# Kernel optimization log

Hardware: AMD Instinct MI355X
Metric: run time of the kernel (lower is better)

The kernel has to match this reference:

```python
import jax, jax.numpy as jnp
import numpy as np

H = 32          # num attention heads
KVH = 8         # num key/value heads
D = 128         # head dim
THETA = 10000.0


def _rope_tables(kv_len):
    inv_freq = 1.0 / (THETA ** (jnp.arange(0, D, 2, dtype=jnp.float32) / D))  # [D/2]
    t = jnp.arange(kv_len, dtype=jnp.float32)
    freqs = jnp.outer(t, inv_freq)                  # [kv_len, D/2]
    emb = jnp.concatenate([freqs, freqs], axis=-1)  # [kv_len, D]
    return jnp.cos(emb), jnp.sin(emb)


def _rotate_half(x):
    x1, x2 = jnp.split(x, 2, axis=-1)
    return jnp.concatenate([-x2, x1], axis=-1)


def setup_inputs() -> dict:
    key = jax.random.key(0)
    ks = jax.random.split(key, 7)
    B, QL, KVL, HID = 4, 128, 4096, 4096
    hidden_states = jax.random.normal(ks[0], (B, QL, HID), jnp.float32)
    key_states = jax.random.normal(ks[1], (B, KVH, KVL, D), jnp.float32)
    value_states = jax.random.normal(ks[2], (B, KVH, KVL, D), jnp.float32)
    Wq = jax.random.normal(ks[3], (HID, H * D), jnp.float32) * (HID ** -0.5)
    Wo = jax.random.normal(ks[4], (H * D, HID), jnp.float32) * ((H * D) ** -0.5)
    position_ids = jnp.sort(jax.random.randint(ks[5], (B, KVL), 0, KVL), axis=-1).astype(jnp.int64)
    attention_mask = jax.random.randint(ks[6], (B, 1, QL, KVL), 0, 2) == 1
    return {"hidden_states": hidden_states, "key_states": key_states,
            "value_states": value_states, "Wq": Wq, "Wo": Wo,
            "position_ids": position_ids, "attention_mask": attention_mask}


def reference(hidden_states, key_states, value_states, Wq, Wo, position_ids, attention_mask):
    B, QL, HID = hidden_states.shape
    KVL = position_ids.shape[-1]

    # q projection -> [B, H, QL, D]
    q = (hidden_states @ Wq).reshape(B, QL, H, D).transpose(0, 2, 1, 3)

    # RoPE: apply rotation for the single max position per batch to all q positions
    cos, sin = _rope_tables(KVL)                               # [KVL, D]
    pos = jnp.take_along_axis(position_ids,
                              jnp.argmax(position_ids.astype(jnp.int32), axis=1)[:, None],
                              axis=1)                          # [B, 1]
    cos_b = cos[pos][:, None]                                  # [B, 1, 1, D]
    sin_b = sin[pos][:, None]
    q = q * cos_b + _rotate_half(q) * sin_b

    # GQA repeat kv heads -> [B, H, KVL, D]
    groups = H // KVH
    k = jnp.repeat(key_states, groups, axis=1)
    v = jnp.repeat(value_states, groups, axis=1)

    scores = jnp.einsum('bhqd,bhkd->bhqk', q, k) / jnp.sqrt(jnp.float32(D))
    scores = jnp.where(attention_mask, jnp.float32(-10000.0), scores)
    attn = jax.nn.softmax(scores.astype(jnp.float32), axis=-1).astype(q.dtype)

    out = jnp.einsum('bhqk,bhkd->bhqd', attn, v)               # [B, H, QL, D]
    out = out.transpose(0, 2, 1, 3).reshape(B, QL, H * D)
    return out @ Wo
```

## Files before the change

### kernel.cpp

```cpp
#include <hip/hip_runtime.h>
#include <math.h>

typedef __attribute__((ext_vector_type(8))) short bf16x8;
typedef __attribute__((ext_vector_type(4))) float f32x4;
typedef __attribute__((ext_vector_type(4))) short s16x4;
typedef __attribute__((ext_vector_type(4))) int i32x4;

__device__ inline unsigned short f2bf(float x){
  unsigned u = __builtin_bit_cast(unsigned, x);
  u = (u + 0x7FFFu + ((u >> 16) & 1u)) >> 16;
  return (unsigned short)u;
}
__device__ inline float bf2f(unsigned short v){
  return __builtin_bit_cast(float, (unsigned)v << 16);
}
__device__ inline unsigned pk2bf(float lo, float hi){
  return (unsigned)f2bf(lo) | ((unsigned)f2bf(hi) << 16);
}

__device__ inline void gl16(const void* g, void* l){
  __builtin_amdgcn_global_load_lds(
      (const __attribute__((address_space(1))) unsigned int*)g,
      (__attribute__((address_space(3))) unsigned int*)l, 16, 0, 0);
}

#define KVLEN 4096
#define QLEN  128
#define NH    32
#define NKVH  8
#define HD    128
#define HIDD  4096
#define NSPLIT 8
#define KVCHUNK (KVLEN / NSPLIT)

__global__ void prep_kernel(const int* __restrict__ pos32,
                            const unsigned int* __restrict__ mask32,
                            float* __restrict__ costab,
                            float* __restrict__ sintab,
                            int* __restrict__ flags){
  int tid = threadIdx.x;
  if (tid < 64){
    unsigned long long bal = __ballot((mask32[tid] & 0xFFFFFF00u) != 0);
    if (tid == 0) flags[0] = (bal != 0) ? 1 : 0;
  }
  int b = tid >> 6, j = tid & 63;
  bool pos64 = (pos32[2*4095 + 1] == 0);
  long long mpos;
  if (pos64) mpos = ((const long long*)pos32)[(size_t)b*KVLEN + KVLEN - 1];
  else       mpos = (long long)pos32[(size_t)b*KVLEN + KVLEN - 1];
  double inv = pow(10000.0, -((double)j) / 64.0);
  double ang = (double)mpos * inv;
  costab[b*64 + j] = (float)cos(ang);
  sintab[b*64 + j] = (float)sin(ang);
}

__global__ __launch_bounds__(256) void maskpack_kernel(const void* __restrict__ mask,
                                                       const int* __restrict__ flags,
                                                       unsigned long long* __restrict__ bits){
  int idx = blockIdx.x * 256 + threadIdx.x;
  bool m8 = (flags[0] != 0);
  bool v = m8 ? (((const unsigned char*)mask)[idx] != 0)
              : (((const int*)mask)[idx] != 0);
  unsigned long long bal = __ballot(v);
  if ((threadIdx.x & 63) == 0) bits[idx >> 6] = bal;
}

__global__ __launch_bounds__(256) void kvprep_kernel(const float* __restrict__ Kg,
                                                     const float* __restrict__ Vg,
                                                     const float* __restrict__ costab,
                                                     const float* __restrict__ sintab,
                                                     unsigned short* __restrict__ Kswz,
                                                     unsigned short* __restrict__ V2){
  __shared__ alignas(16) char tl[16384];
  int bid = blockIdx.x;
  int tid = threadIdx.x;
  int b = bid >> 9;
  const float* kin = Kg + (size_t)bid * 8192;
  const float* vin = Vg + (size_t)bid * 8192;
  unsigned short* kout = Kswz + (size_t)bid * 8192;
  unsigned short* vout = V2   + (size_t)bid * 8192;
#pragma unroll
  for (int i = 0; i < 4; ++i){
    int c = tid + 256*i;
    int r = c >> 4, d0 = (c & 15) * 8;
    int dp = d0 ^ 64;
    bool low = d0 < 64;
    f32x4 x0 = *(const f32x4*)(kin + r*128 + d0);
    f32x4 x1 = *(const f32x4*)(kin + r*128 + d0 + 4);
    f32x4 y0 = *(const f32x4*)(kin + r*128 + dp);
    f32x4 y1 = *(const f32x4*)(kin + r*128 + dp + 4);
    int j0 = d0 & 63;
    bf16x8 s;
#pragma unroll
    for (int t = 0; t < 4; ++t){
      float cc = costab[b*64 + j0 + t],     ss = sintab[b*64 + j0 + t];
      float c2 = costab[b*64 + j0 + 4 + t], s2 = sintab[b*64 + j0 + 4 + t];
      float v0 = low ? (x0[t]*cc + y0[t]*ss) : (x0[t]*cc - y0[t]*ss);
      float v1 = low ? (x1[t]*c2 + y1[t]*s2) : (x1[t]*c2 - y1[t]*s2);
      s[t] = (short)f2bf(v0);
      s[t+4] = (short)f2bf(v1);
    }
    unsigned o = ((unsigned)(r*256 + d0*2)) ^ (((unsigned)r & 7u) << 4);
    *(bf16x8*)(tl + o) = s;
  }
  __syncthreads();
#pragma unroll
  for (int i = 0; i < 4; ++i)
    *(bf16x8*)((char*)kout + tid*16 + i*4096) = *(const bf16x8*)(tl + tid*16 + i*4096);
#pragma unroll
  for (int i = 0; i < 4; ++i){
    int c = tid + 256*i;
    int l16 = c & 15, lk4 = (c >> 4) & 3, ks2 = (c >> 6) & 1, nf8 = c >> 7;
    int d = nf8*16 + l16;
    int kvb = ks2*32 + lk4*8;
    bf16x8 s;
#pragma unroll
    for (int e = 0; e < 8; ++e) s[e] = (short)f2bf(vin[(size_t)(kvb + e)*128 + d]);
    *(bf16x8*)(vout + (size_t)c*8) = s;
  }
}

__global__ __launch_bounds__(256) void wprep_kernel(const float* __restrict__ Wq,
                                                    const float* __restrict__ Wo,
                                                    const float* __restrict__ hidden,
                                                    unsigned short* __restrict__ WqImg,
                                                    unsigned short* __restrict__ WoImg,
                                                    unsigned short* __restrict__ A1img){
  __shared__ alignas(16) char tl[8192];
  int bid = blockIdx.x, tid = threadIdx.x;
  if (bid < 8192){
    const float* W = (bid < 4096) ? Wq : Wo;
    unsigned short* img = (bid < 4096) ? WqImg : WoImg;
    int t = bid & 4095;
    int bn = t >> 6, kt = t & 63;
    char* outB = (char*)img + (size_t)t * 8192;
#pragma unroll
    for (int i = 0; i < 2; ++i){
      int c = tid + 256*i;
      int n = c & 63, kc = c >> 6;
      const float* src = W + (size_t)(kt*64 + kc*8) * HIDD + bn*64 + n;
      bf16x8 s;
#pragma unroll
      for (int e = 0; e < 8; ++e) s[e] = (short)f2bf(src[(size_t)e * HIDD]);
      unsigned off = ((unsigned)(n*128 + kc*16)) ^ (((unsigned)n & 7u) << 4);
      *(bf16x8*)(tl + off) = s;
    }
    __syncthreads();
#pragma unroll
    for (int i = 0; i < 2; ++i)
      *(bf16x8*)(outB + tid*16 + i*4096) = *(const bf16x8*)(tl + tid*16 + i*4096);
  } else {
    int t = bid - 8192;
    int bm = t >> 6, kt = t & 63;
    char* outA = (char*)A1img + (size_t)t * 8192;
#pragma unroll
    for (int i = 0; i < 2; ++i){
      int c = tid + 256*i;
      int m = c >> 3, kc = c & 7;
      const float* src = hidden + (size_t)(bm*64 + m) * HIDD + kt*64 + kc*8;
      f32x4 x0 = *(const f32x4*)src;
      f32x4 x1 = *(const f32x4*)(src + 4);
      bf16x8 s;
#pragma unroll
      for (int e = 0; e < 4; ++e){ s[e] = (short)f2bf(x0[e]); s[e+4] = (short)f2bf(x1[e]); }
      unsigned off = ((unsigned)(m*128 + kc*16)) ^ (((unsigned)m & 7u) << 4);
      *(bf16x8*)(tl + off) = s;
    }
    __syncthreads();
#pragma unroll
    for (int i = 0; i < 2; ++i)
      *(bf16x8*)(outA + tid*16 + i*4096) = *(const bf16x8*)(tl + tid*16 + i*4096);
  }
}

template<int EPI>
__global__ __launch_bounds__(256, 2) void gemm_kernel(const unsigned short* __restrict__ Aimg,
                                                      const unsigned short* __restrict__ Bimg,
                                                      void* __restrict__ C_){
  __shared__ alignas(16) char smem[65536];
  int bid = blockIdx.x;
  int bn = (bid & 7) | ((bid >> 6) << 3);
  int bm = (bid >> 3) & 7;
  int tid = threadIdx.x, lane = tid & 63, w = tid >> 6;
  int wm = w >> 1, wn = w & 1;
  int l16 = lane & 15, lk4 = lane >> 4;
  const char* At = (const char*)Aimg + (size_t)(bm*64) * 8192;
  const char* Bt = (const char*)Bimg + (size_t)(bn*64) * 8192;
  f32x4 acc[2][2] = {};

#define GSTAGE(KT, BUF) do { \
    const char* ga_ = At + (size_t)(KT)*8192 + w*2048 + lane*16; \
    const char* gb_ = Bt + (size_t)(KT)*8192 + w*2048 + lane*16; \
    char* la_ = smem + (BUF)*16384 + w*2048; \
    char* lb_ = smem + (BUF)*16384 + 8192 + w*2048; \
    gl16(ga_, la_); gl16(ga_ + 1024, la_ + 1024); \
    gl16(gb_, lb_); gl16(gb_ + 1024, lb_ + 1024); \
  } while(0)

  GSTAGE(0, 0); GSTAGE(1, 1); GSTAGE(2, 2);

  for (int kt = 0; kt < 64; ++kt){
    if (kt < 62)      asm volatile("s_waitcnt vmcnt(8)" ::: "memory");
    else if (kt < 63) asm volatile("s_waitcnt vmcnt(4)" ::: "memory");
    else              asm volatile("s_waitcnt vmcnt(0)" ::: "memory");
    asm volatile("s_waitcnt lgkmcnt(0)" ::: "memory");
    __builtin_amdgcn_s_barrier();
    __builtin_amdgcn_sched_barrier(0);
    if (kt + 3 < 64) GSTAGE(kt + 3, (kt + 3) & 3);
    const char* Ab = smem + (kt & 3)*16384;
    const char* Bb = Ab + 8192;
    bf16x8 af[2][2], bfr[2][2];
#pragma unroll
    for (int i = 0; i < 2; ++i)
#pragma unroll
      for (int ks = 0; ks < 2; ++ks){
        unsigned m = (unsigned)(wm*32 + i*16 + l16);
        unsigned off = (m*128u + (unsigned)(ks*64 + lk4*16)) ^ ((m & 7u) << 4);
        af[i][ks] = *(const bf16x8*)(Ab + off);
      }
#pragma unroll
    for (int j = 0; j < 2; ++j)
#pragma unroll
      for (int ks = 0; ks < 2; ++ks){
        unsigned n = (unsigned)(wn*32 + j*16 + l16);
        unsigned off = (n*128u + (unsigned)(ks*64 + lk4*16)) ^ ((n & 7u) << 4);
        bfr[j][ks] = *(const bf16x8*)(Bb + off);
      }
#pragma unroll
    for (int i = 0; i < 2; ++i)
#pragma unroll
      for (int j = 0; j < 2; ++j)
#pragma unroll
        for (int ks = 0; ks < 2; ++ks)
          acc[i][j] = __builtin_amdgcn_mfma_f32_16x16x32_bf16(af[i][ks], bfr[j][ks], acc[i][j], 0, 0, 0);
  }
#undef GSTAGE

  if (EPI == 0){
    float* C = (float*)C_;
#pragma unroll
    for (int i = 0; i < 2; ++i)
#pragma unroll
      for (int j = 0; j < 2; ++j)
#pragma unroll
        for (int r = 0; r < 4; ++r){
          int row = bm*64 + wm*32 + i*16 + lk4*4 + r;
          int col = bn*64 + wn*32 + j*16 + l16;
          C[(size_t)row * HIDD + col] = acc[i][j][r];
        }
  } else {
    unsigned short* Q = (unsigned short*)C_;
    const float scale = 0.08838834764831845f * 1.4426950408889634f;
#pragma unroll
    for (int i = 0; i < 2; ++i)
#pragma unroll
      for (int j = 0; j < 2; ++j)
#pragma unroll
        for (int r = 0; r < 4; ++r){
          int row = bm*64 + wm*32 + i*16 + lk4*4 + r;
          int col = bn*64 + wn*32 + j*16 + l16;
          int b = row >> 7, ql = row & 127;
          int h = col >> 7, d = col & 127;
          Q[(((size_t)(b*NH + h)) * QLEN + ql) * HD + d] = f2bf(acc[i][j][r] * scale);
        }
  }
}

__global__ __launch_bounds__(256, 2) void attn_kernel(const unsigned short* __restrict__ Q,
                                                      const unsigned short* __restrict__ Kswz,
                                                      const unsigned short* __restrict__ V2,
                                                      const unsigned long long* __restrict__ bits,
                                                      unsigned short* __restrict__ Opart,
                                                      float* __restrict__ Mpart,
                                                      float* __restrict__ Lpart){
  __shared__ alignas(16) unsigned short Kbuf[2][8192];
  __shared__ alignas(16) unsigned short Vbuf[2][8192];
  int bid = blockIdx.x;
  int j = (bid >> 3) & 3;
  int g = (bid & 7) | ((bid >> 5) << 3);
  int s   = g & 7;
  int kvh = (g >> 3) & 7;
  int b   = g >> 6;
  int h   = kvh * 4 + j;

  int tid = threadIdx.x, lane = tid & 63, w = tid >> 6;
  int l16 = lane & 15, lk4 = lane >> 4;
  int lk4x4 = lk4 * 4;

  bf16x8 qf[2][4];
#pragma unroll
  for (int qg = 0; qg < 2; ++qg){
    const unsigned short* qp = Q + (((size_t)(b*NH + h) * QLEN) + w*32 + qg*16 + l16) * HD;
#pragma unroll
    for (int ks = 0; ks < 4; ++ks)
      qf[qg][ks] = *(const bf16x8*)(qp + ks*32 + lk4*8);
  }
  bf16x8 vone;
#pragma unroll
  for (int t = 0; t < 8; ++t) vone[t] = (short)0x3F80;

  f32x4 acc_o[2][8] = {};
  f32x4 acc_l[2] = {};
  float mrun[2] = {-1e30f, -1e30f};

  size_t kvhbase = (size_t)(b*NKVH + kvh) * (KVLEN/64);
  const unsigned short* Ktiles = Kswz + kvhbase * 8192;
  const unsigned short* Vtiles = V2   + kvhbase * 8192;
  size_t qrow0 = (size_t)(b*QLEN + w*32 + l16);

  const int t0 = s * (KVCHUNK/64), t1 = t0 + KVCHUNK/64;
  int srcb0 = (l16 + ((lk4 & 1) << 5)) << 2;
  int srcb1 = srcb0 + 64;

#define STAGE(T, BUF) do { \
    const char* gk_ = (const char*)(Ktiles + (size_t)(T)*8192) + w*4096 + lane*16; \
    const char* gv_ = (const char*)(Vtiles + (size_t)(T)*8192) + w*4096 + lane*16; \
    char* lk_ = (char*)(&Kbuf[BUF][0]) + w*4096; \
    char* lv_ = (char*)(&Vbuf[BUF][0]) + w*4096; \
    _Pragma("unroll") for (int i_ = 0; i_ < 4; ++i_) gl16(gk_ + i_*1024, lk_ + i_*1024); \
    _Pragma("unroll") for (int i_ = 0; i_ < 4; ++i_) gl16(gv_ + i_*1024, lv_ + i_*1024); \
  } while(0)

  STAGE(t0, 0);
  int cur = 0;
  for (int t = t0; t < t1; ++t){
    asm volatile("s_waitcnt vmcnt(0)" ::: "memory");
    asm volatile("s_waitcnt lgkmcnt(0)" ::: "memory");
    __builtin_amdgcn_s_barrier();
    __builtin_amdgcn_sched_barrier(0);
    if (t + 1 < t1) STAGE(t + 1, cur ^ 1);

    unsigned long long wrd[2];
    wrd[0] = bits[qrow0*64 + (size_t)t];
    wrd[1] = bits[(qrow0 + 16)*64 + (size_t)t];

    const char* Kc = (const char*)&Kbuf[cur][0];
    const char* Vc = (const char*)&Vbuf[cur][0];

    f32x4 sacc[2][4] = {};
#pragma unroll
    for (int nf = 0; nf < 4; ++nf){
      int krow = nf*16 + l16;
#pragma unroll
      for (int ks = 0; ks < 4; ++ks){
        unsigned byteoff = ((unsigned)krow*256u + (unsigned)(ks*32 + lk4*8)*2u) ^ (((unsigned)krow & 7u) << 4);
        bf16x8 kf = *(const bf16x8*)(Kc + byteoff);
        sacc[0][nf] = __builtin_amdgcn_mfma_f32_16x16x32_bf16(kf, qf[0][ks], sacc[0][nf], 0, 0, 0);
        sacc[1][nf] = __builtin_amdgcn_mfma_f32_16x16x32_bf16(kf, qf[1][ks], sacc[1][nf], 0, 0, 0);
      }
    }

    unsigned P32[2][8];
#pragma unroll
    for (int qg = 0; qg < 2; ++qg){
      float pp[4][4];
      float pm = -1e30f;
#pragma unroll
      for (int nf = 0; nf < 4; ++nf)
#pragma unroll
        for (int r = 0; r < 4; ++r){
          bool mk = (wrd[qg] >> (nf*16 + lk4x4 + r)) & 1ull;
          float sv = mk ? -20000.f : sacc[qg][nf][r];
          pp[nf][r] = sv;
          pm = fmaxf(pm, sv);
        }
      pm = fmaxf(pm, __shfl_xor(pm, 16, 64));
      pm = fmaxf(pm, __shfl_xor(pm, 32, 64));
      if (__any(pm > mrun[qg])){
        float mnew = fmaxf(mrun[qg], pm);
        float corr = exp2f(mrun[qg] - mnew);
        mrun[qg] = mnew;
#pragma unroll
        for (int nf8 = 0; nf8 < 8; ++nf8)
#pragma unroll
          for (int r = 0; r < 4; ++r) acc_o[qg][nf8][r] *= corr;
#pragma unroll
        for (int r = 0; r < 4; ++r) acc_l[qg][r] *= corr;
      }
#pragma unroll
      for (int nf = 0; nf < 4; ++nf){
        float e0 = exp2f(pp[nf][0] - mrun[qg]);
        float e1 = exp2f(pp[nf][1] - mrun[qg]);
        float e2 = exp2f(pp[nf][2] - mrun[qg]);
        float e3 = exp2f(pp[nf][3] - mrun[qg]);
        P32[qg][nf*2]     = pk2bf(e0, e1);
        P32[qg][nf*2 + 1] = pk2bf(e2, e3);
      }
    }

    bf16x8 pf[2][2];
    bool hi = lk4 >= 2;
#pragma unroll
    for (int qg = 0; qg < 2; ++qg)
#pragma unroll
      for (int ks2 = 0; ks2 < 2; ++ks2){
        int a0 = __builtin_amdgcn_ds_bpermute(srcb0, (int)P32[qg][ks2*4 + 0]);
        int b0 = __builtin_amdgcn_ds_bpermute(srcb0, (int)P32[qg][ks2*4 + 2]);
        int a1 = __builtin_amdgcn_ds_bpermute(srcb0, (int)P32[qg][ks2*4 + 1]);
        int b1 = __builtin_amdgcn_ds_bpermute(srcb0, (int)P32[qg][ks2*4 + 3]);
        int a2 = __builtin_amdgcn_ds_bpermute(srcb1, (int)P32[qg][ks2*4 + 0]);
        int b2 = __builtin_amdgcn_ds_bpermute(srcb1, (int)P32[qg][ks2*4 + 2]);
        int a3 = __builtin_amdgcn_ds_bpermute(srcb1, (int)P32[qg][ks2*4 + 1]);
        int b3 = __builtin_amdgcn_ds_bpermute(srcb1, (int)P32[qg][ks2*4 + 3]);
        i32x4 wv = { hi ? b0 : a0, hi ? b1 : a1, hi ? b2 : a2, hi ? b3 : a3 };
        pf[qg][ks2] = __builtin_bit_cast(bf16x8, wv);
      }

#pragma unroll
    for (int nf8 = 0; nf8 < 8; ++nf8)
#pragma unroll
      for (int ks2 = 0; ks2 < 2; ++ks2){
        unsigned byteoff = (unsigned)(nf8*2 + ks2)*1024u + (unsigned)lane*16u;
        bf16x8 vf = *(const bf16x8*)(Vc + byteoff);
        acc_o[0][nf8] = __builtin_amdgcn_mfma_f32_16x16x32_bf16(vf, pf[0][ks2], acc_o[0][nf8], 0, 0, 0);
        acc_o[1][nf8] = __builtin_amdgcn_mfma_f32_16x16x32_bf16(vf, pf[1][ks2], acc_o[1][nf8], 0, 0, 0);
      }
#pragma unroll
    for (int qg = 0; qg < 2; ++qg)
#pragma unroll
      for (int ks2 = 0; ks2 < 2; ++ks2)
        acc_l[qg] = __builtin_amdgcn_mfma_f32_16x16x32_bf16(vone, pf[qg][ks2], acc_l[qg], 0, 0, 0);

    cur ^= 1;
  }
#undef STAGE

  size_t rowbase = ((size_t)(s*4 + b) * NH + h) * QLEN + w*32 + l16;
#pragma unroll
  for (int qg = 0; qg < 2; ++qg){
    size_t row = rowbase + qg*16;
#pragma unroll
    for (int nf8 = 0; nf8 < 8; ++nf8){
      s16x4 o;
#pragma unroll
      for (int r = 0; r < 4; ++r) o[r] = (short)f2bf(acc_o[qg][nf8][r]);
      *(s16x4*)&Opart[row * HD + nf8*16 + lk4x4] = o;
    }
    if (lk4 == 0){
      Mpart[row] = mrun[qg];
      Lpart[row] = acc_l[qg][0];
    }
  }
}

__global__ __launch_bounds__(256) void combine_kernel(const unsigned short* __restrict__ Opart,
                                                      const float* __restrict__ Mpart,
                                                      const float* __restrict__ Lpart,
                                                      unsigned short* __restrict__ A2img){
  int idx = blockIdx.x * 256 + threadIdx.x;
  int d4 = idx & 31;
  int row = idx >> 5;
  const int RS = 4 * NH * QLEN;
  float m[NSPLIT];
  float M = -1e30f;
#pragma unroll
  for (int s = 0; s < NSPLIT; ++s){
    m[s] = Mpart[(size_t)s*RS + row];
    M = fmaxf(M, m[s]);
  }
  float L = 0.f;
  f32x4 num = {};
#pragma unroll
  for (int s = 0; s < NSPLIT; ++s){
    float wsc = exp2f(m[s] - M);
    L += wsc * Lpart[(size_t)s*RS + row];
    s16x4 o = *(const s16x4*)&Opart[((size_t)s*RS + row) * HD + d4*4];
#pragma unroll
    for (int t = 0; t < 4; ++t) num[t] += wsc * bf2f((unsigned short)o[t]);
  }
  int ql = row & 127, h = (row >> 7) & 31, b = row >> 12;
  int bm = b*2 + (ql >> 6), mm = ql & 63;
  int kt = h*2 + (d4 >> 4), kl = (d4*4) & 63;
  s16x4 res;
#pragma unroll
  for (int t = 0; t < 4; ++t) res[t] = (short)f2bf(num[t] / L);
  char* tile = (char*)A2img + (size_t)(bm*64 + kt) * 8192;
  unsigned off = ((unsigned)(mm*128 + kl*2)) ^ (((unsigned)mm & 7u) << 4);
  *(s16x4*)(tile + off) = res;
}

extern "C" void kernel_launch(void* const* d_in, const int* in_sizes, int n_in,
                              void* d_out, int out_size, void* d_ws, size_t ws_size,
                              hipStream_t stream){
  (void)in_sizes; (void)n_in; (void)out_size; (void)ws_size;
  const float* hidden = (const float*)d_in[0];
  const float* kst    = (const float*)d_in[1];
  const float* vst    = (const float*)d_in[2];
  const float* wq     = (const float*)d_in[3];
  const float* wo     = (const float*)d_in[4];
  const void*  pos    = d_in[5];
  const void*  mask   = d_in[6];
  float* out = (float*)d_out;

  char* ws = (char*)d_ws;
  unsigned short* Kswz  = (unsigned short*)ws;
  unsigned short* V2    = (unsigned short*)(ws + (32u << 20));
  unsigned short* WoImg = (unsigned short*)(ws + (64u << 20));
  unsigned short* WqImg = (unsigned short*)(ws + (96u << 20));
  unsigned short* Opart = (unsigned short*)(ws + (96u << 20));
  unsigned short* A1img = (unsigned short*)(ws + (128u << 20));
  unsigned short* qbf   = (unsigned short*)(ws + (132u << 20));
  unsigned short* A2img = (unsigned short*)(ws + (136u << 20));
  float* Mpart = (float*)(ws + (140u << 20));
  float* Lpart = (float*)(ws + (140u << 20) + (512u << 10));
  unsigned long long* bits = (unsigned long long*)(ws + (141u << 20));
  float* costab = (float*)(ws + (141u << 20) + (256u << 10));
  float* sintab = costab + 256;
  int*   flags  = (int*)(sintab + 256);

  prep_kernel<<<1, 256, 0, stream>>>((const int*)pos, (const unsigned int*)mask,
                                     costab, sintab, flags);
  maskpack_kernel<<<8192, 256, 0, stream>>>(mask, flags, bits);
  kvprep_kernel<<<2048, 256, 0, stream>>>(kst, vst, costab, sintab, Kswz, V2);
  wprep_kernel<<<8704, 256, 0, stream>>>(wq, wo, hidden, WqImg, WoImg, A1img);
  gemm_kernel<1><<<512, 256, 0, stream>>>(A1img, WqImg, qbf);
  attn_kernel<<<1024, 256, 0, stream>>>(qbf, Kswz, V2, bits, Opart, Mpart, Lpart);
  combine_kernel<<<2048, 256, 0, stream>>>(Opart, Mpart, Lpart, A2img);
  gemm_kernel<0><<<512, 256, 0, stream>>>(A2img, WoImg, out);
}
```

Before: 230.6 us.

## Fuse prep kernels into one launch, deepen GEMM k-step, halve attention splits

Merges the four preprocessing kernels (rope table, mask packing, K/V conversion, weight/hidden conversion) into a single launch, computing RoPE sin/cos inline per element instead of from a precomputed table. This removes several launch gaps and serial dependencies. The GEMM now double-buffers 128-wide k-tiles instead of triple/quad-buffering 64-wide ones, which halves the number of barriers but makes the prefetch shallower. The attention KV split count drops from 8 to 4, so fewer blocks and less partial-result traffic go into combine, at the cost of lower parallelism.

```diff
diff --git a/kernel.cpp b/kernel.cpp
--- a/kernel.cpp
+++ b/kernel.cpp
@@ -30,146 +30,128 @@
 #define NKVH  8
 #define HD    128
 #define HIDD  4096
-#define NSPLIT 8
+#define NSPLIT 4
 #define KVCHUNK (KVLEN / NSPLIT)
 
-__global__ void prep_kernel(const int* __restrict__ pos32,
-                            const unsigned int* __restrict__ mask32,
-                            float* __restrict__ costab,
-                            float* __restrict__ sintab,
-                            int* __restrict__ flags){
-  int tid = threadIdx.x;
-  if (tid < 64){
-    unsigned long long bal = __ballot((mask32[tid] & 0xFFFFFF00u) != 0);
-    if (tid == 0) flags[0] = (bal != 0) ? 1 : 0;
-  }
-  int b = tid >> 6, j = tid & 63;
-  bool pos64 = (pos32[2*4095 + 1] == 0);
-  long long mpos;
-  if (pos64) mpos = ((const long long*)pos32)[(size_t)b*KVLEN + KVLEN - 1];
-  else       mpos = (long long)pos32[(size_t)b*KVLEN + KVLEN - 1];
-  double inv = pow(10000.0, -((double)j) / 64.0);
-  double ang = (double)mpos * inv;
-  costab[b*64 + j] = (float)cos(ang);
-  sintab[b*64 + j] = (float)sin(ang);
-}
-
-__global__ __launch_bounds__(256) void maskpack_kernel(const void* __restrict__ mask,
-                                                       const int* __restrict__ flags,
-                                                       unsigned long long* __restrict__ bits){
-  int idx = blockIdx.x * 256 + threadIdx.x;
-  bool m8 = (flags[0] != 0);
-  bool v = m8 ? (((const unsigned char*)mask)[idx] != 0)
-              : (((const int*)mask)[idx] != 0);
-  unsigned long long bal = __ballot(v);
-  if ((threadIdx.x & 63) == 0) bits[idx >> 6] = bal;
-}
-
-__global__ __launch_bounds__(256) void kvprep_kernel(const float* __restrict__ Kg,
-                                                     const float* __restrict__ Vg,
-                                                     const float* __restrict__ costab,
-                                                     const float* __restrict__ sintab,
-                                                     unsigned short* __restrict__ Kswz,
-                                                     unsigned short* __restrict__ V2){
+__global__ __launch_bounds__(256) void prepall_kernel(
+    const float* __restrict__ Kg, const float* __restrict__ Vg,
+    const float* __restrict__ Wq, const float* __restrict__ Wo,
+    const float* __restrict__ hidden, const void* __restrict__ mask,
+    const int* __restrict__ pos32,
+    unsigned short* __restrict__ Kswz, unsigned short* __restrict__ V2,
+    unsigned short* __restrict__ WqImg, unsigned short* __restrict__ WoImg,
+    unsigned short* __restrict__ A1img,
+    unsigned long long* __restrict__ bits){
   __shared__ alignas(16) char tl[16384];
-  int bid = blockIdx.x;
-  int tid = threadIdx.x;
-  int b = bid >> 9;
-  const float* kin = Kg + (size_t)bid * 8192;
-  const float* vin = Vg + (size_t)bid * 8192;
-  unsigned short* kout = Kswz + (size_t)bid * 8192;
-  unsigned short* vout = V2   + (size_t)bid * 8192;
-#pragma unroll
-  for (int i = 0; i < 4; ++i){
-    int c = tid + 256*i;
-    int r = c >> 4, d0 = (c & 15) * 8;
-    int dp = d0 ^ 64;
-    bool low = d0 < 64;
-    f32x4 x0 = *(const f32x4*)(kin + r*128 + d0);
-    f32x4 x1 = *(const f32x4*)(kin + r*128 + d0 + 4);
-    f32x4 y0 = *(const f32x4*)(kin + r*128 + dp);
-    f32x4 y1 = *(const f32x4*)(kin + r*128 + dp + 4);
-    int j0 = d0 & 63;
-    bf16x8 s;
-#pragma unroll
-    for (int t = 0; t < 4; ++t){
-      float cc = costab[b*64 + j0 + t],     ss = sintab[b*64 + j0 + t];
-      float c2 = costab[b*64 + j0 + 4 + t], s2 = sintab[b*64 + j0 + 4 + t];
-      float v0 = low ? (x0[t]*cc + y0[t]*ss) : (x0[t]*cc - y0[t]*ss);
-      float v1 = low ? (x1[t]*c2 + y1[t]*s2) : (x1[t]*c2 - y1[t]*s2);
-      s[t] = (short)f2bf(v0);
-      s[t+4] = (short)f2bf(v1);
-    }
-    unsigned o = ((unsigned)(r*256 + d0*2)) ^ (((unsigned)r & 7u) << 4);
-    *(bf16x8*)(tl + o) = s;
-  }
-  __syncthreads();
-#pragma unroll
-  for (int i = 0; i < 4; ++i)
-    *(bf16x8*)((char*)kout + tid*16 + i*4096) = *(const bf16x8*)(tl + tid*16 + i*4096);
-#pragma unroll
-  for (int i = 0; i < 4; ++i){
-    int c = tid + 256*i;
-    int l16 = c & 15, lk4 = (c >> 4) & 3, ks2 = (c >> 6) & 1, nf8 = c >> 7;
-    int d = nf8*16 + l16;
-    int kvb = ks2*32 + lk4*8;
-    bf16x8 s;
-#pragma unroll
-    for (int e = 0; e < 8; ++e) s[e] = (short)f2bf(vin[(size_t)(kvb + e)*128 + d]);
-    *(bf16x8*)(vout + (size_t)c*8) = s;
-  }
-}
-
-__global__ __launch_bounds__(256) void wprep_kernel(const float* __restrict__ Wq,
-                                                    const float* __restrict__ Wo,
-                                                    const float* __restrict__ hidden,
-                                                    unsigned short* __restrict__ WqImg,
-                                                    unsigned short* __restrict__ WoImg,
-                                                    unsigned short* __restrict__ A1img){
-  __shared__ alignas(16) char tl[8192];
   int bid = blockIdx.x, tid = threadIdx.x;
+
   if (bid < 8192){
-    const float* W = (bid < 4096) ? Wq : Wo;
-    unsigned short* img = (bid < 4096) ? WqImg : WoImg;
-    int t = bid & 4095;
-    int bn = t >> 6, kt = t & 63;
-    char* outB = (char*)img + (size_t)t * 8192;
-#pragma unroll
-    for (int i = 0; i < 2; ++i){
+    const unsigned int* m32 = (const unsigned int*)mask;
+    unsigned long long det = __ballot((m32[tid & 63] & 0xFFFFFF00u) != 0);
+    bool m8 = (det != 0);
+    int idx = bid * 256 + tid;
+    bool v = m8 ? (((const unsigned char*)mask)[idx] != 0)
+                : (((const int*)mask)[idx] != 0);
+    unsigned long long bal = __ballot(v);
+    if ((tid & 63) == 0) bits[idx >> 6] = bal;
+
+  } else if (bid < 10240){
+    int t = bid - 8192;
+    int b = t >> 9;
+    const float* kin = Kg + (size_t)t * 8192;
+    const float* vin = Vg + (size_t)t * 8192;
+    unsigned short* kout = Kswz + (size_t)t * 8192;
+    unsigned short* vout = V2   + (size_t)t * 8192;
+    bool pos64 = (pos32[2*4095 + 1] == 0);
+    float mpos;
+    if (pos64) mpos = (float)((const long long*)pos32)[(size_t)b*KVLEN + KVLEN - 1];
+    else       mpos = (float)pos32[(size_t)b*KVLEN + KVLEN - 1];
+    const float KC = -0.2076205059298351f;
+#pragma unroll
+    for (int i = 0; i < 4; ++i){
       int c = tid + 256*i;
-      int n = c & 63, kc = c >> 6;
-      const float* src = W + (size_t)(kt*64 + kc*8) * HIDD + bn*64 + n;
+      int r = c >> 4, d0 = (c & 15) * 8;
+      int dp = d0 ^ 64;
+      bool low = d0 < 64;
+      f32x4 x0 = *(const f32x4*)(kin + r*128 + d0);
+      f32x4 x1 = *(const f32x4*)(kin + r*128 + d0 + 4);
+      f32x4 y0 = *(const f32x4*)(kin + r*128 + dp);
+      f32x4 y1 = *(const f32x4*)(kin + r*128 + dp + 4);
+      int j0 = d0 & 63;
       bf16x8 s;
 #pragma unroll
-      for (int e = 0; e < 8; ++e) s[e] = (short)f2bf(src[(size_t)e * HIDD]);
-      unsigned off = ((unsigned)(n*128 + kc*16)) ^ (((unsigned)n & 7u) << 4);
-      *(bf16x8*)(tl + off) = s;
+      for (int tt = 0; tt < 8; ++tt){
+        float ss, cc;
+        sincosf(mpos * exp2f((float)(j0 + tt) * KC), &ss, &cc);
+        float x = (tt < 4) ? x0[tt] : x1[tt-4];
+        float y = (tt < 4) ? y0[tt] : y1[tt-4];
+        float v = low ? (x*cc + y*ss) : (x*cc - y*ss);
+        s[tt] = (short)f2bf(v);
+      }
+      unsigned o = ((unsigned)(r*256 + d0*2)) ^ (((unsigned)r & 7u) << 4);
+      *(bf16x8*)(tl + o) = s;
     }
     __syncthreads();
 #pragma unroll
-    for (int i = 0; i < 2; ++i)
-      *(bf16x8*)(outB + tid*16 + i*4096) = *(const bf16x8*)(tl + tid*16 + i*4096);
+    for (int i = 0; i < 4; ++i)
+      *(bf16x8*)((char*)kout + tid*16 + i*4096) = *(const bf16x8*)(tl + tid*16 + i*4096);
+#pragma unroll
+    for (int i = 0; i < 4; ++i){
+      int c = tid + 256*i;
+      int l16 = c & 15, lk4 = (c >> 4) & 3, ks2 = (c >> 6) & 1, nf8 = c >> 7;
+      int d = nf8*16 + l16;
+      int kvb = ks2*32 + lk4*8;
+      bf16x8 s;
+#pragma unroll
+      for (int e = 0; e < 8; ++e) s[e] = (short)f2bf(vin[(size_t)(kvb + e)*128 + d]);
+      *(bf16x8*)(vout + (size_t)c*8) = s;
+    }
+
   } else {
-    int t = bid - 8192;
-    int bm = t >> 6, kt = t & 63;
-    char* outA = (char*)A1img + (size_t)t * 8192;
-#pragma unroll
-    for (int i = 0; i < 2; ++i){
-      int c = tid + 256*i;
-      int m = c >> 3, kc = c & 7;
-      const float* src = hidden + (size_t)(bm*64 + m) * HIDD + kt*64 + kc*8;
-      f32x4 x0 = *(const f32x4*)src;
-      f32x4 x1 = *(const f32x4*)(src + 4);
-      bf16x8 s;
-#pragma unroll
-      for (int e = 0; e < 4; ++e){ s[e] = (short)f2bf(x0[e]); s[e+4] = (short)f2bf(x1[e]); }
-      unsigned off = ((unsigned)(m*128 + kc*16)) ^ (((unsigned)m & 7u) << 4);
-      *(bf16x8*)(tl + off) = s;
-    }
-    __syncthreads();
-#pragma unroll
-    for (int i = 0; i < 2; ++i)
-      *(bf16x8*)(outA + tid*16 + i*4096) = *(const bf16x8*)(tl + tid*16 + i*4096);
+    int t = bid - 10240;
+    if (t < 8192){
+      const float* W = (t < 4096) ? Wq : Wo;
+      unsigned short* img = (t < 4096) ? WqImg : WoImg;
+      int tt = t & 4095;
+      int bn = tt >> 6, kt = tt & 63;
+      char* outB = (char*)img + (size_t)tt * 8192;
+#pragma unroll
+      for (int i = 0; i < 2; ++i){
+        int c = tid + 256*i;
+        int n = c & 63, kc = c >> 6;
+        const float* src = W + (size_t)(kt*64 + kc*8) * HIDD + bn*64 + n;
+        bf16x8 s;
+#pragma unroll
+        for (int e = 0; e < 8; ++e) s[e] = (short)f2bf(src[(size_t)e * HIDD]);
+        unsigned off = ((unsigned)(n*128 + kc*16)) ^ (((unsigned)n & 7u) << 4);
+        *(bf16x8*)(tl + off) = s;
+      }
+      __syncthreads();
+#pragma unroll
+      for (int i = 0; i < 2; ++i)
+        *(bf16x8*)(outB + tid*16 + i*4096) = *(const bf16x8*)(tl + tid*16 + i*4096);
+    } else {
+      int ta = t - 8192;
+      int bm = ta >> 6, kt = ta & 63;
+      char* outA = (char*)A1img + (size_t)ta * 8192;
+#pragma unroll
+      for (int i = 0; i < 2; ++i){
+        int c = tid + 256*i;
+        int m = c >> 3, kc = c & 7;
+        const float* src = hidden + (size_t)(bm*64 + m) * HIDD + kt*64 + kc*8;
+        f32x4 x0 = *(const f32x4*)src;
+        f32x4 x1 = *(const f32x4*)(src + 4);
+        bf16x8 s;
+#pragma unroll
+        for (int e = 0; e < 4; ++e){ s[e] = (short)f2bf(x0[e]); s[e+4] = (short)f2bf(x1[e]); }
+        unsigned off = ((unsigned)(m*128 + kc*16)) ^ (((unsigned)m & 7u) << 4);
+        *(bf16x8*)(tl + off) = s;
+      }
+      __syncthreads();
+#pragma unroll
+      for (int i = 0; i < 2; ++i)
+        *(bf16x8*)(outA + tid*16 + i*4096) = *(const bf16x8*)(tl + tid*16 + i*4096);
+    }
   }
 }
 
@@ -188,42 +170,42 @@
   const char* Bt = (const char*)Bimg + (size_t)(bn*64) * 8192;
   f32x4 acc[2][2] = {};
 
-#define GSTAGE(KT, BUF) do { \
-    const char* ga_ = At + (size_t)(KT)*8192 + w*2048 + lane*16; \
-    const char* gb_ = Bt + (size_t)(KT)*8192 + w*2048 + lane*16; \
-    char* la_ = smem + (BUF)*16384 + w*2048; \
-    char* lb_ = smem + (BUF)*16384 + 8192 + w*2048; \
-    gl16(ga_, la_); gl16(ga_ + 1024, la_ + 1024); \
-    gl16(gb_, lb_); gl16(gb_ + 1024, lb_ + 1024); \
+#define GSTAGE(KT2, BUF) do { \
+    const char* ga_ = At + (size_t)(KT2)*16384 + w*4096 + lane*16; \
+    const char* gb_ = Bt + (size_t)(KT2)*16384 + w*4096 + lane*16; \
+    char* la_ = smem + (BUF)*32768 + w*4096; \
+    char* lb_ = smem + (BUF)*32768 + 16384 + w*4096; \
+    _Pragma("unroll") for (int i_ = 0; i_ < 4; ++i_) gl16(ga_ + i_*1024, la_ + i_*1024); \
+    _Pragma("unroll") for (int i_ = 0; i_ < 4; ++i_) gl16(gb_ + i_*1024, lb_ + i_*1024); \
   } while(0)
 
-  GSTAGE(0, 0); GSTAGE(1, 1); GSTAGE(2, 2);
-
-  for (int kt = 0; kt < 64; ++kt){
-    if (kt < 62)      asm volatile("s_waitcnt vmcnt(8)" ::: "memory");
-    else if (kt < 63) asm volatile("s_waitcnt vmcnt(4)" ::: "memory");
-    else              asm volatile("s_waitcnt vmcnt(0)" ::: "memory");
+  GSTAGE(0, 0);
+
+  for (int kt = 0; kt < 32; ++kt){
+    asm volatile("s_waitcnt vmcnt(0)" ::: "memory");
     asm volatile("s_waitcnt lgkmcnt(0)" ::: "memory");
     __builtin_amdgcn_s_barrier();
     __builtin_amdgcn_sched_barrier(0);
-    if (kt + 3 < 64) GSTAGE(kt + 3, (kt + 3) & 3);
-    const char* Ab = smem + (kt & 3)*16384;
-    const char* Bb = Ab + 8192;
-    bf16x8 af[2][2], bfr[2][2];
+    if (kt + 1 < 32) GSTAGE(kt + 1, (kt + 1) & 1);
+    const char* Ab = smem + (kt & 1)*32768;
+    const char* Bb = Ab + 16384;
+    bf16x8 af[2][4], bfr[2][4];
 #pragma unroll
     for (int i = 0; i < 2; ++i)
 #pragma unroll
-      for (int ks = 0; ks < 2; ++ks){
+      for (int ks = 0; ks < 4; ++ks){
         unsigned m = (unsigned)(wm*32 + i*16 + l16);
-        unsigned off = (m*128u + (unsigned)(ks*64 + lk4*16)) ^ ((m & 7u) << 4);
+        unsigned off = (unsigned)(ks >> 1)*8192u +
+                       ((m*128u + (unsigned)((ks & 1)*64 + lk4*16)) ^ ((m & 7u) << 4));
         af[i][ks] = *(const bf16x8*)(Ab + off);
       }
 #pragma unroll
     for (int j = 0; j < 2; ++j)
 #pragma unroll
-      for (int ks = 0; ks < 2; ++ks){
+      for (int ks = 0; ks < 4; ++ks){
         unsigned n = (unsigned)(wn*32 + j*16 + l16);
-        unsigned off = (n*128u + (unsigned)(ks*64 + lk4*16)) ^ ((n & 7u) << 4);
+        unsigned off = (unsigned)(ks >> 1)*8192u +
+                       ((n*128u + (unsigned)((ks & 1)*64 + lk4*16)) ^ ((n & 7u) << 4));
         bfr[j][ks] = *(const bf16x8*)(Bb + off);
       }
 #pragma unroll
@@ -231,7 +213,7 @@
 #pragma unroll
       for (int j = 0; j < 2; ++j)
 #pragma unroll
-        for (int ks = 0; ks < 2; ++ks)
+        for (int ks = 0; ks < 4; ++ks)
           acc[i][j] = __builtin_amdgcn_mfma_f32_16x16x32_bf16(af[i][ks], bfr[j][ks], acc[i][j], 0, 0, 0);
   }
 #undef GSTAGE
@@ -278,9 +260,9 @@
   int bid = blockIdx.x;
   int j = (bid >> 3) & 3;
   int g = (bid & 7) | ((bid >> 5) << 3);
-  int s   = g & 7;
-  int kvh = (g >> 3) & 7;
-  int b   = g >> 6;
+  int s   = g & 3;
+  int kvh = (g >> 2) & 7;
+  int b   = g >> 5;
   int h   = kvh * 4 + j;
 
   int tid = threadIdx.x, lane = tid & 63, w = tid >> 6;
@@ -502,19 +484,14 @@
   unsigned short* qbf   = (unsigned short*)(ws + (132u << 20));
   unsigned short* A2img = (unsigned short*)(ws + (136u << 20));
   float* Mpart = (float*)(ws + (140u << 20));
-  float* Lpart = (float*)(ws + (140u << 20) + (512u << 10));
-  unsigned long long* bits = (unsigned long long*)(ws + (141u << 20));
-  float* costab = (float*)(ws + (141u << 20) + (256u << 10));
-  float* sintab = costab + 256;
-  int*   flags  = (int*)(sintab + 256);
-
-  prep_kernel<<<1, 256, 0, stream>>>((const int*)pos, (const unsigned int*)mask,
-                                     costab, sintab, flags);
-  maskpack_kernel<<<8192, 256, 0, stream>>>(mask, flags, bits);
-  kvprep_kernel<<<2048, 256, 0, stream>>>(kst, vst, costab, sintab, Kswz, V2);
-  wprep_kernel<<<8704, 256, 0, stream>>>(wq, wo, hidden, WqImg, WoImg, A1img);
+  float* Lpart = (float*)(ws + (140u << 20) + (256u << 10));
+  unsigned long long* bits = (unsigned long long*)(ws + (140u << 20) + (512u << 10));
+
+  prepall_kernel<<<18944, 256, 0, stream>>>(kst, vst, wq, wo, hidden, mask,
+                                            (const int*)pos,
+                                            Kswz, V2, WqImg, WoImg, A1img, bits);
   gemm_kernel<1><<<512, 256, 0, stream>>>(A1img, WqImg, qbf);
-  attn_kernel<<<1024, 256, 0, stream>>>(qbf, Kswz, V2, bits, Opart, Mpart, Lpart);
+  attn_kernel<<<512, 256, 0, stream>>>(qbf, Kswz, V2, bits, Opart, Mpart, Lpart);
   combine_kernel<<<2048, 256, 0, stream>>>(Opart, Mpart, Lpart, A2img);
   gemm_kernel<0><<<512, 256, 0, stream>>>(A2img, WoImg, out);
 }
```

New measurement: 217.4 us. 5.7% less time.
